# Performance work log

Hardware: AMD Instinct MI355X
Metric: run time of the kernel (lower is better)

The kernel has to match this reference:

```python
import jax, jax.numpy as jnp
import numpy as np

DX = float(np.sqrt(512.0))  # fixed scale from the module (self.dx = sqrt(512))


def setup_inputs() -> dict:
    key = jax.random.key(0)
    ks = jax.random.split(key, 6)
    B, C, H, W = 4, 512, 64, 64
    Cq = C // 32  # reduce=32 -> 16 q/k channels
    q = jax.random.normal(ks[0], (B, C, H, W), dtype=jnp.float32)
    k = jax.random.normal(ks[1], (B, C, H, W), dtype=jnp.float32)
    v = jax.random.normal(ks[2], (B, C, H, W), dtype=jnp.float32)
    # 1x1 conv weights, kaiming-ish scale
    wq = jax.random.normal(ks[3], (Cq, C), dtype=jnp.float32) / np.sqrt(C)
    wk = jax.random.normal(ks[4], (Cq, C), dtype=jnp.float32) / np.sqrt(C)
    wv = jax.random.normal(ks[5], (C, C), dtype=jnp.float32) / np.sqrt(C)
    bq = jnp.zeros((Cq,), dtype=jnp.float32)
    bk = jnp.zeros((Cq,), dtype=jnp.float32)
    bv = jnp.zeros((C,), dtype=jnp.float32)
    return {"q": q, "k": k, "v": v, "wq": wq, "bq": bq, "wk": wk, "bk": bk, "wv": wv, "bv": bv}


def reference(q, k, v, wq, bq, wk, bk, wv, bv):
    B, C, H, W = q.shape
    N = H * W
    # 1x1 convs == per-pixel channel matmuls; flatten spatial to N tokens
    qf = q.reshape(B, C, N)
    kf = k.reshape(B, C, N)
    vf = v.reshape(B, C, N)
    proj_q = jnp.einsum('oc,bcn->bno', wq, qf) + bq  # [B, N, Cq]
    proj_k = jnp.einsum('oc,bcn->bon', wk, kf) + bk[:, None]  # [B, Cq, N]
    proj_v = jnp.einsum('oc,bcn->bon', wv, vf) + bv[:, None]  # [B, C, N]
    # energy[b,i,j] = <proj_q[b,i], proj_k[b,:,j]>
    energy = jnp.einsum('bid,bdj->bij', proj_q, proj_k)  # [B, N, N]
    attention = jax.nn.softmax(energy / DX, axis=-1)
    # out[b,c,i] = sum_j proj_v[b,c,j] * attention[b,i,j]
    out = jnp.einsum('bcj,bij->bci', proj_v, attention)
    return out.reshape(B, C, H, W) + v
```

## Files before the change

kernel.cpp:

```cpp
#include <hip/hip_runtime.h>
#include <hip/hip_bf16.h>

typedef __bf16 bf16;
typedef __bf16 bf16x8 __attribute__((ext_vector_type(8)));
typedef float f32x16 __attribute__((ext_vector_type(16)));
typedef float f32x4 __attribute__((ext_vector_type(4)));
typedef unsigned int u32x4 __attribute__((ext_vector_type(4)));

#define NB 4
#define NC 512
#define NN 4096

static constexpr float EXP2_SCALE = 0.063763926f;

static __device__ __forceinline__ unsigned pack_bf2(float a, float b){
  unsigned short ux = __builtin_bit_cast(unsigned short, (bf16)a);
  unsigned short uy = __builtin_bit_cast(unsigned short, (bf16)b);
  return (unsigned)ux | ((unsigned)uy << 16);
}

union FragU { unsigned u[4]; bf16x8 v; };

static __device__ __forceinline__ f32x16 zero16(){
  f32x16 z;
#pragma unroll
  for(int i=0;i<16;i++) z[i] = 0.0f;
  return z;
}

__global__ __launch_bounds__(256) void k_wv_cvt(const float* __restrict__ wv,
                                                bf16* __restrict__ wvL){
  int t  = blockIdx.x * 256 + threadIdx.x;
  int cg = t & 31;
  int co = t >> 5;
  const float* s = wv + (size_t)co * NC + cg * 16;
  unsigned w[8];
#pragma unroll
  for(int j=0;j<8;j++) w[j] = pack_bf2(s[2*j], s[2*j+1]);
  u32x4* d = (u32x4*)((char*)wvL + (size_t)(cg * NC + co) * 32);
  d[0] = (u32x4){w[0],w[1],w[2],w[3]};
  d[1] = (u32x4){w[4],w[5],w[6],w[7]};
}

__global__ __launch_bounds__(256) void k_v_cvt(const float* __restrict__ v,
                                               bf16* __restrict__ vL){
  int bid = blockIdx.x;
  int n  = (bid & 15) * 256 + threadIdx.x;
  int cg = (bid >> 4) & 31;
  int b  = bid >> 9;
  const float* s = v + ((size_t)(b * NC + cg * 16)) * NN + n;
  unsigned w[8];
#pragma unroll
  for(int j=0;j<8;j++) w[j] = pack_bf2(s[(size_t)(2*j)*NN], s[(size_t)(2*j+1)*NN]);
  u32x4* d = (u32x4*)((char*)vL + ((size_t)(b*32 + cg) * NN + n) * 32);
  d[0] = (u32x4){w[0],w[1],w[2],w[3]};
  d[1] = (u32x4){w[4],w[5],w[6],w[7]};
}

__global__ __launch_bounds__(512) void k_proj_qk(
    const float* __restrict__ q, const float* __restrict__ kin,
    const float* __restrict__ wq, const float* __restrict__ bq,
    const float* __restrict__ wk, const float* __restrict__ bk,
    bf16* __restrict__ Pq, bf16* __restrict__ Pk){
  __shared__ float red[8][64][20];
  int b  = blockIdx.x >> 6;
  int n0 = (blockIdx.x & 63) * 64;
  int w  = threadIdx.x >> 6;
  int lane = threadIdx.x & 63;
  int isk = w >> 2;
  const float* src = isk ? kin : q;
  const float* wt  = isk ? wk : wq;
  int c0 = (w & 3) * 128;
  float acc[16];
#pragma unroll
  for(int o=0;o<16;o++) acc[o] = 0.0f;
  const float* sp = src + ((size_t)(b * NC + c0)) * NN + n0 + lane;
#pragma unroll 4
  for(int c=0;c<128;c++){
    float x = sp[(size_t)c * NN];
#pragma unroll
    for(int o=0;o<16;o++) acc[o] += wt[o * NC + c0 + c] * x;
  }
#pragma unroll
  for(int o4=0;o4<4;o4++)
    *(f32x4*)&red[w][lane][o4*4] = (f32x4){acc[o4*4],acc[o4*4+1],acc[o4*4+2],acc[o4*4+3]};
  __syncthreads();
  if(threadIdx.x < 128){
    int wk2 = threadIdx.x >> 6;
    int tok = threadIdx.x & 63;
    const float* bias = wk2 ? bk : bq;
    bf16* dst = wk2 ? Pk : Pq;
    int wb = wk2 * 4;
    unsigned wd[8];
#pragma unroll
    for(int t=0;t<8;t++){
      float a0 = bias[2*t],  a1 = bias[2*t+1];
#pragma unroll
      for(int ww=0;ww<4;ww++){
        a0 += red[wb+ww][tok][2*t];
        a1 += red[wb+ww][tok][2*t+1];
      }
      wd[t] = pack_bf2(a0, a1);
    }
    u32x4* d = (u32x4*)((char*)dst + ((size_t)(b * NN + n0 + tok)) * 32);
    d[0] = (u32x4){wd[0],wd[1],wd[2],wd[3]};
    d[1] = (u32x4){wd[4],wd[5],wd[6],wd[7]};
  }
}

__global__ __launch_bounds__(256) void k_proj_v(
    const bf16* __restrict__ wvL, const bf16* __restrict__ vL,
    const float* __restrict__ bv, bf16* __restrict__ PvL){
  int bid = blockIdx.x;
  int nt  = bid & 63;
  int cot = (bid >> 6) & 7;
  int b   = bid >> 9;
  int w    = threadIdx.x >> 6;
  int lane = threadIdx.x & 63;
  int l31 = lane & 31, h = lane >> 5;
  int co0 = cot * 64 + (w >> 1) * 32;
  int n0  = nt * 64 + (w & 1) * 32;
  const char* ap = (const char*)wvL + (size_t)(co0 + l31) * 32 + h * 16;
  const char* bp = (const char*)vL + ((size_t)(b * 32) * NN + n0 + l31) * 32 + h * 16;
  f32x16 acc = zero16();
  for(int kc=0;kc<32;kc++){
    bf16x8 af  = *(const bf16x8*)(ap + (size_t)kc * NC * 32);
    bf16x8 bfr = *(const bf16x8*)(bp + (size_t)kc * NN * 32);
    acc = __builtin_amdgcn_mfma_f32_32x32x16_bf16(af, bfr, acc, 0, 0, 0);
  }
  int j = n0 + l31;
  char* dbase = (char*)PvL + ((size_t)(b*256 + (j >> 4)) * NC) * 32 + (j & 15) * 2;
#pragma unroll
  for(int r=0;r<16;r++){
    int row = (r & 3) + 8 * (r >> 2) + 4 * h;
    int co = co0 + row;
    float val = acc[r] + bv[co];
    *(bf16*)(dbase + (size_t)co * 32) = (bf16)val;
  }
}

__global__ __launch_bounds__(512, 4) void k_attn(
    const bf16* __restrict__ Pq, const bf16* __restrict__ Pk,
    const bf16* __restrict__ PvL, const float* __restrict__ vin,
    float* __restrict__ out){
  __shared__ __attribute__((aligned(16))) unsigned P_lds[2][8][64][8];
  __shared__ float lsum_lds[8][64];
  int blk  = blockIdx.x;
  int xcd  = blk & 7;
  int b    = xcd >> 1;
  int itile= ((blk >> 3) << 1) | (xcd & 1);
  int i0 = itile * 32;
  int w    = threadIdx.x >> 6;
  int lane = threadIdx.x & 63;
  int l31 = lane & 31, h = lane >> 5;
  int c0 = w * 64;
  int sw4 = ((lane >> 2) & 1) * 4;

  bf16x8 qf = *(const bf16x8*)((const char*)Pq + ((size_t)(b * NN + i0 + l31)) * 32 + h * 16);

  f32x16 acc0 = zero16(), acc1 = zero16();
  float lsum = 0.0f;

  const char* pkbase = (const char*)Pk  + ((size_t)b * NN) * 32 + h * 16;
  const char* pvbase = (const char*)PvL + ((size_t)(b * 256) * NC) * 32 + h * 16;

  bf16x8 kf = *(const bf16x8*)(pkbase + (size_t)(w * 32 + l31) * 32);

  for(int J=0;J<16;J++){
    int buf = J & 1;
    {
      f32x16 s = __builtin_amdgcn_mfma_f32_32x32x16_bf16(kf, qf, zero16(), 0, 0, 0);
      if(J < 15)
        kf = *(const bf16x8*)(pkbase + (size_t)((J+1)*8*32 + w*32 + l31) * 32);
      float p[16];
#pragma unroll
      for(int r=0;r<16;r++){ p[r] = exp2f(s[r] * EXP2_SCALE); lsum += p[r]; }
      unsigned qw[8], ew[8];
#pragma unroll
      for(int t=0;t<8;t++) qw[t] = pack_bf2(p[2*t], p[2*t+1]);
#pragma unroll
      for(int t=0;t<8;t++) ew[t] = (unsigned)__shfl_xor((int)qw[t], 32);
      u32x4 pa0 = h ? (u32x4){ew[2],ew[3],qw[2],qw[3]} : (u32x4){qw[0],qw[1],ew[0],ew[1]};
      u32x4 pa1 = h ? (u32x4){ew[6],ew[7],qw[6],qw[7]} : (u32x4){qw[4],qw[5],ew[4],ew[5]};
      unsigned* row = &P_lds[buf][w][lane][0];
      *(u32x4*)(row + sw4)       = pa0;
      *(u32x4*)(row + (4 - sw4)) = pa1;
    }
    __syncthreads();
#pragma unroll
    for(int t=0;t<8;t++){
      FragU pa0, pa1;
      const unsigned* row = &P_lds[buf][t][lane][0];
      *(u32x4*)pa0.u = *(const u32x4*)(row + sw4);
      *(u32x4*)pa1.u = *(const u32x4*)(row + (4 - sw4));
      const char* pvp = pvbase + (((size_t)(J*8 + t) * 2) * NC + c0 + l31) * 32;
      bf16x8 v00 = *(const bf16x8*)(pvp);
      bf16x8 v10 = *(const bf16x8*)(pvp + (size_t)NC * 32);
      bf16x8 v01 = *(const bf16x8*)(pvp + 1024);
      bf16x8 v11 = *(const bf16x8*)(pvp + (size_t)NC * 32 + 1024);
      acc0 = __builtin_amdgcn_mfma_f32_32x32x16_bf16(pa0.v, v00, acc0, 0, 0, 0);
      acc0 = __builtin_amdgcn_mfma_f32_32x32x16_bf16(pa1.v, v10, acc0, 0, 0, 0);
      acc1 = __builtin_amdgcn_mfma_f32_32x32x16_bf16(pa0.v, v01, acc1, 0, 0, 0);
      acc1 = __builtin_amdgcn_mfma_f32_32x32x16_bf16(pa1.v, v11, acc1, 0, 0, 0);
    }
  }
  lsum_lds[w][lane] = lsum;
  __syncthreads();
  float rowsum = 0.0f;
#pragma unroll
  for(int ww=0;ww<8;ww++) rowsum += lsum_lds[ww][l31] + lsum_lds[ww][l31 + 32];
  float rl = 1.0f / rowsum;
  float rlr[16];
#pragma unroll
  for(int r=0;r<16;r++) rlr[r] = __shfl(rl, (r & 3) + 8 * (r >> 2) + 4 * h);
#pragma unroll
  for(int cs=0;cs<2;cs++){
    f32x16 a = cs ? acc1 : acc0;
    int c = c0 + cs * 32 + l31;
    const float* vp = vin + ((size_t)(b * NC + c)) * NN + i0;
    float* op = out + ((size_t)(b * NC + c)) * NN + i0;
#pragma unroll
    for(int g=0;g<4;g++){
      int ib = 8 * g + 4 * h;
      f32x4 vv = *(const f32x4*)(vp + ib);
      f32x4 ov;
#pragma unroll
      for(int e=0;e<4;e++) ov[e] = a[4*g+e] * rlr[4*g+e] + vv[e];
      *(f32x4*)(op + ib) = ov;
    }
  }
}

extern "C" void kernel_launch(void* const* d_in, const int* in_sizes, int n_in,
                              void* d_out, int out_size, void* d_ws, size_t ws_size,
                              hipStream_t stream) {
  const float* q  = (const float*)d_in[0];
  const float* k  = (const float*)d_in[1];
  const float* v  = (const float*)d_in[2];
  const float* wq = (const float*)d_in[3];
  const float* bq = (const float*)d_in[4];
  const float* wk = (const float*)d_in[5];
  const float* bk = (const float*)d_in[6];
  const float* wv = (const float*)d_in[7];
  const float* bv = (const float*)d_in[8];
  float* out = (float*)d_out;
  char* ws = (char*)d_ws;

  bf16* Pq  = (bf16*)(ws);
  bf16* Pk  = (bf16*)(ws + (1u<<19));
  bf16* wvL = (bf16*)(ws + (2u<<19));
  bf16* vL  = (bf16*)(ws + (3u<<19));
  bf16* PvL = (bf16*)(ws + (3u<<19) + (16u<<20));

  k_wv_cvt <<<64,   256, 0, stream>>>(wv, wvL);
  k_v_cvt  <<<2048, 256, 0, stream>>>(v, vL);
  k_proj_qk<<<256,  512, 0, stream>>>(q, k, wq, bq, wk, bk, Pq, Pk);
  k_proj_v <<<2048, 256, 0, stream>>>(wvL, vL, bv, PvL);
  k_attn   <<<512,  512, 0, stream>>>(Pq, Pk, PvL, v, out);
}
```

Baseline: 315.7 us.

## Prefetch V fragments, fold softmax scale into Q, coalesce Pv stores

The exp2 scale is folded into the Q projection, removing a multiply per score. The V-projection output is staged through shared memory so each lane writes two 16-byte vectors instead of scattered bf16 stores. The attention loop now double-buffers V fragments in registers two steps ahead. It also uses permlane32_swap instead of shuffles, replaces __syncthreads with a raw barrier after an lgkmcnt wait, and raises wave priority around the MFMAs. The cost is extra registers, which may hurt occupancy at 4 waves per SIMD, and Q loses a little precision because the scale is applied before the bf16 rounding.

```diff
diff --git a/kernel.cpp b/kernel.cpp
--- a/kernel.cpp
+++ b/kernel.cpp
@@ -90,6 +90,7 @@
     int tok = threadIdx.x & 63;
     const float* bias = wk2 ? bk : bq;
     bf16* dst = wk2 ? Pk : Pq;
+    float sc = wk2 ? 1.0f : EXP2_SCALE;
     int wb = wk2 * 4;
     unsigned wd[8];
 #pragma unroll
@@ -100,7 +101,7 @@
         a0 += red[wb+ww][tok][2*t];
         a1 += red[wb+ww][tok][2*t+1];
       }
-      wd[t] = pack_bf2(a0, a1);
+      wd[t] = pack_bf2(a0 * sc, a1 * sc);
     }
     u32x4* d = (u32x4*)((char*)dst + ((size_t)(b * NN + n0 + tok)) * 32);
     d[0] = (u32x4){wd[0],wd[1],wd[2],wd[3]};
@@ -111,6 +112,7 @@
 __global__ __launch_bounds__(256) void k_proj_v(
     const bf16* __restrict__ wvL, const bf16* __restrict__ vL,
     const float* __restrict__ bv, bf16* __restrict__ PvL){
+  __shared__ float stg[4][2][33][17];
   int bid = blockIdx.x;
   int nt  = bid & 63;
   int cot = (bid >> 6) & 7;
@@ -128,15 +130,18 @@
     bf16x8 bfr = *(const bf16x8*)(bp + (size_t)kc * NN * 32);
     acc = __builtin_amdgcn_mfma_f32_32x32x16_bf16(af, bfr, acc, 0, 0, 0);
   }
-  int j = n0 + l31;
-  char* dbase = (char*)PvL + ((size_t)(b*256 + (j >> 4)) * NC) * 32 + (j & 15) * 2;
 #pragma unroll
   for(int r=0;r<16;r++){
     int row = (r & 3) + 8 * (r >> 2) + 4 * h;
-    int co = co0 + row;
-    float val = acc[r] + bv[co];
-    *(bf16*)(dbase + (size_t)co * 32) = (bf16)val;
-  }
+    stg[w][l31 >> 4][row][l31 & 15] = acc[r] + bv[co0 + row];
+  }
+  const float* rp = &stg[w][lane >> 5][l31][0];
+  unsigned wd[8];
+#pragma unroll
+  for(int jl=0;jl<8;jl++) wd[jl] = pack_bf2(rp[2*jl], rp[2*jl+1]);
+  char* gb = (char*)PvL + (((size_t)(b*256 + (n0 >> 4) + (lane >> 5))) * NC + co0 + l31) * 32;
+  *(u32x4*)gb        = (u32x4){wd[0],wd[1],wd[2],wd[3]};
+  *(u32x4*)(gb + 16) = (u32x4){wd[4],wd[5],wd[6],wd[7]};
 }
 
 __global__ __launch_bounds__(512, 4) void k_attn(
@@ -159,11 +164,21 @@
   bf16x8 qf = *(const bf16x8*)((const char*)Pq + ((size_t)(b * NN + i0 + l31)) * 32 + h * 16);
 
   f32x16 acc0 = zero16(), acc1 = zero16();
-  float lsum = 0.0f;
+  f32x4 lsv = (f32x4){0.f, 0.f, 0.f, 0.f};
 
   const char* pkbase = (const char*)Pk  + ((size_t)b * NN) * 32 + h * 16;
   const char* pvbase = (const char*)PvL + ((size_t)(b * 256) * NC) * 32 + h * 16;
 
+#define PVP(T) (pvbase + ((size_t)(T) * 2 * NC + c0 + l31) * 32)
+  bf16x8 vb[2][4];
+#pragma unroll
+  for(int s0=0;s0<2;s0++){
+    const char* p0 = PVP(s0);
+    vb[s0][0] = *(const bf16x8*)(p0);
+    vb[s0][1] = *(const bf16x8*)(p0 + (size_t)NC * 32);
+    vb[s0][2] = *(const bf16x8*)(p0 + 1024);
+    vb[s0][3] = *(const bf16x8*)(p0 + (size_t)NC * 32 + 1024);
+  }
   bf16x8 kf = *(const bf16x8*)(pkbase + (size_t)(w * 32 + l31) * 32);
 
   for(int J=0;J<16;J++){
@@ -174,36 +189,54 @@
         kf = *(const bf16x8*)(pkbase + (size_t)((J+1)*8*32 + w*32 + l31) * 32);
       float p[16];
 #pragma unroll
-      for(int r=0;r<16;r++){ p[r] = exp2f(s[r] * EXP2_SCALE); lsum += p[r]; }
-      unsigned qw[8], ew[8];
+      for(int r=0;r<16;r++){ p[r] = exp2f(s[r]); lsv[r & 3] += p[r]; }
+      unsigned qw[8];
 #pragma unroll
       for(int t=0;t<8;t++) qw[t] = pack_bf2(p[2*t], p[2*t+1]);
+      u32x4 pa0, pa1;
+#if __has_builtin(__builtin_amdgcn_permlane32_swap)
+      auto r0 = __builtin_amdgcn_permlane32_swap(qw[0], qw[2], false, false);
+      auto r1 = __builtin_amdgcn_permlane32_swap(qw[1], qw[3], false, false);
+      auto r2 = __builtin_amdgcn_permlane32_swap(qw[4], qw[6], false, false);
+      auto r3 = __builtin_amdgcn_permlane32_swap(qw[5], qw[7], false, false);
+      pa0 = (u32x4){(unsigned)r0[0], (unsigned)r1[0], (unsigned)r0[1], (unsigned)r1[1]};
+      pa1 = (u32x4){(unsigned)r2[0], (unsigned)r3[0], (unsigned)r2[1], (unsigned)r3[1]};
+#else
+      unsigned ew[8];
 #pragma unroll
       for(int t=0;t<8;t++) ew[t] = (unsigned)__shfl_xor((int)qw[t], 32);
-      u32x4 pa0 = h ? (u32x4){ew[2],ew[3],qw[2],qw[3]} : (u32x4){qw[0],qw[1],ew[0],ew[1]};
-      u32x4 pa1 = h ? (u32x4){ew[6],ew[7],qw[6],qw[7]} : (u32x4){qw[4],qw[5],ew[4],ew[5]};
+      pa0 = h ? (u32x4){ew[2],ew[3],qw[2],qw[3]} : (u32x4){qw[0],qw[1],ew[0],ew[1]};
+      pa1 = h ? (u32x4){ew[6],ew[7],qw[6],qw[7]} : (u32x4){qw[4],qw[5],ew[4],ew[5]};
+#endif
       unsigned* row = &P_lds[buf][w][lane][0];
       *(u32x4*)(row + sw4)       = pa0;
       *(u32x4*)(row + (4 - sw4)) = pa1;
     }
-    __syncthreads();
+    asm volatile("s_waitcnt lgkmcnt(0)" ::: "memory");
+    __builtin_amdgcn_s_barrier();
+    asm volatile("" ::: "memory");
 #pragma unroll
     for(int t=0;t<8;t++){
       FragU pa0, pa1;
       const unsigned* row = &P_lds[buf][t][lane][0];
       *(u32x4*)pa0.u = *(const u32x4*)(row + sw4);
       *(u32x4*)pa1.u = *(const u32x4*)(row + (4 - sw4));
-      const char* pvp = pvbase + (((size_t)(J*8 + t) * 2) * NC + c0 + l31) * 32;
-      bf16x8 v00 = *(const bf16x8*)(pvp);
-      bf16x8 v10 = *(const bf16x8*)(pvp + (size_t)NC * 32);
-      bf16x8 v01 = *(const bf16x8*)(pvp + 1024);
-      bf16x8 v11 = *(const bf16x8*)(pvp + (size_t)NC * 32 + 1024);
-      acc0 = __builtin_amdgcn_mfma_f32_32x32x16_bf16(pa0.v, v00, acc0, 0, 0, 0);
-      acc0 = __builtin_amdgcn_mfma_f32_32x32x16_bf16(pa1.v, v10, acc0, 0, 0, 0);
-      acc1 = __builtin_amdgcn_mfma_f32_32x32x16_bf16(pa0.v, v01, acc1, 0, 0, 0);
-      acc1 = __builtin_amdgcn_mfma_f32_32x32x16_bf16(pa1.v, v11, acc1, 0, 0, 0);
-    }
-  }
+      __builtin_amdgcn_s_setprio(1);
+      acc0 = __builtin_amdgcn_mfma_f32_32x32x16_bf16(pa0.v, vb[t & 1][0], acc0, 0, 0, 0);
+      acc0 = __builtin_amdgcn_mfma_f32_32x32x16_bf16(pa1.v, vb[t & 1][1], acc0, 0, 0, 0);
+      acc1 = __builtin_amdgcn_mfma_f32_32x32x16_bf16(pa0.v, vb[t & 1][2], acc1, 0, 0, 0);
+      acc1 = __builtin_amdgcn_mfma_f32_32x32x16_bf16(pa1.v, vb[t & 1][3], acc1, 0, 0, 0);
+      __builtin_amdgcn_s_setprio(0);
+      int Tn = J * 8 + t + 2; if(Tn > 127) Tn = 127;
+      const char* pn = PVP(Tn);
+      vb[t & 1][0] = *(const bf16x8*)(pn);
+      vb[t & 1][1] = *(const bf16x8*)(pn + (size_t)NC * 32);
+      vb[t & 1][2] = *(const bf16x8*)(pn + 1024);
+      vb[t & 1][3] = *(const bf16x8*)(pn + (size_t)NC * 32 + 1024);
+    }
+  }
+#undef PVP
+  float lsum = (lsv[0] + lsv[1]) + (lsv[2] + lsv[3]);
   lsum_lds[w][lane] = lsum;
   __syncthreads();
   float rowsum = 0.0f;
```

Measured after the change: 309.7 us. Within noise of the previous version (-1.9%).
